# Kernel tuning notes

Measured on AMD Instinct MI355X. Metric: run time of the kernel, lower is better.

## Reference

```python
import jax, jax.numpy as jnp
import numpy as np
from jax.scipy.ndimage import map_coordinates

ANGLES = 180
PROJ = 180
IMG = 256
THETA_RAD = np.deg2rad(np.linspace(0.0, 180.0, ANGLES, endpoint=False)).astype(np.float32)


def _ramp_filter(size):
    # skimage _get_fourier_filter(size, 'ramp')
    n = np.concatenate((np.arange(1, size // 2 + 1, 2),
                        np.arange(size // 2 - 1, 0, -2)))
    f = np.zeros(size)
    f[0] = 0.25
    f[1::2] = -1.0 / (np.pi * n) ** 2
    return (2.0 * np.real(np.fft.fft(f))).astype(np.float32)


def radon_t(img, theta):
    # skimage radon(circle=True): rotate by each angle (bilinear warp) and sum rows
    N = img.shape[0]
    center = N // 2
    y, x = jnp.mgrid[0:N, 0:N]
    x = x.astype(jnp.float32)
    y = y.astype(jnp.float32)

    def one(th):
        c, s = jnp.cos(th), jnp.sin(th)
        sx = c * x + s * y - center * (c + s - 1.0)   # source col
        sy = -s * x + c * y - center * (c - s - 1.0)  # source row
        rot = map_coordinates(img, [sy, sx], order=1, mode='constant', cval=0.0)
        return rot.sum(axis=0)  # sum over rows -> [N]

    cols = jax.vmap(one)(theta)  # [A, N]
    return cols.T                # [N, A] sinogram


def iradon_t(sino, theta):
    # skimage iradon(circle=True, filter='ramp', interpolation='linear')
    N, A = sino.shape
    pad = max(64, int(2 ** np.ceil(np.log2(2 * N))))
    filt = jnp.asarray(_ramp_filter(pad))
    proj = jnp.fft.fft(jnp.pad(sino, ((0, pad - N), (0, 0))), axis=0) * filt[:, None]
    filtered = jnp.real(jnp.fft.ifft(proj, axis=0)[:N, :]).astype(jnp.float32)  # [N, A]

    radius = N // 2
    xpr, ypr = jnp.mgrid[0:N, 0:N]
    xpr = (xpr - radius).astype(jnp.float32)
    ypr = (ypr - radius).astype(jnp.float32)

    def one(col, th):
        # detector coordinate t, shifted so index 0 corresponds to x[0] = -N//2
        t = ypr * jnp.cos(th) - xpr * jnp.sin(th) + radius
        i0 = jnp.floor(t).astype(jnp.int32)
        frac = t - i0
        v0 = col[jnp.clip(i0, 0, N - 1)]
        v1 = col[jnp.clip(i0 + 1, 0, N - 1)]
        val = (1.0 - frac) * v0 + frac * v1
        inb = (t >= 0.0) & (t <= N - 1.0)  # np.interp(..., left=0, right=0)
        return jnp.where(inb, val, 0.0)

    back = jax.vmap(one)(filtered.T, theta).sum(axis=0)  # [N, N]
    mask = (xpr ** 2 + ypr ** 2) <= radius ** 2
    return jnp.where(mask, back, 0.0) * (jnp.pi / (2.0 * A))


def setup_inputs() -> dict:
    key = jax.random.key(0)
    ks = jax.random.split(key, 7)
    scale = 1.0 / np.sqrt(PROJ)
    return {
        "x": jax.random.normal(ks[0], (4, 3, IMG, IMG), dtype=jnp.float32),
        "Wq": jax.random.normal(ks[1], (PROJ, PROJ), dtype=jnp.float32) * scale,
        "bq": jax.random.normal(ks[2], (PROJ,), dtype=jnp.float32) * scale,
        "Wk": jax.random.normal(ks[3], (PROJ, PROJ), dtype=jnp.float32) * scale,
        "bk": jax.random.normal(ks[4], (PROJ,), dtype=jnp.float32) * scale,
        "Wv": jax.random.normal(ks[5], (PROJ, PROJ), dtype=jnp.float32) * scale,
        "bv": jax.random.normal(ks[6], (PROJ,), dtype=jnp.float32) * scale,
    }


def reference(x, Wq, bq, Wk, bk, Wv, bv):
    B, C, H, W = x.shape
    theta = jnp.asarray(THETA_RAD)
    imgs = x.reshape(B * C, H, W)
    sino = jax.vmap(lambda im: radon_t(im, theta))(imgs)  # [BC, H, A]
    Q = sino @ Wq.T + bq
    K = sino @ Wk.T + bk
    V = sino @ Wv.T + bv
    scores = jax.nn.softmax(
        jnp.einsum('nij,nkj->nik', Q, K) / jnp.sqrt(jnp.float32(PROJ)), axis=-1)
    att = jnp.einsum('nik,nkj->nij', scores, V)            # [BC, H, A]
    rec = jax.vmap(lambda s: iradon_t(s, theta))(att)      # [BC, H, W]
    return rec.reshape(B, C, H, W)
```

## Files before the change

### kernel.cpp

```cpp
#include <hip/hip_runtime.h>

#define AANG 180
#define NN 256
#define BCH 12

#ifndef M_PI
#define M_PI 3.14159265358979323846
#endif

__device__ __forceinline__ int iclamp(int v, int lo, int hi) {
    return v < lo ? lo : (v > hi ? hi : v);
}

#define LSTR 259
#define LROWSMAX 130

__global__ __launch_bounds__(1024, 1)
void radon_kernel(const float* __restrict__ x, float* __restrict__ partial) {
    __shared__ float tile[LROWSMAX * LSTR];
    __shared__ float red[2][1024];
    int blk = blockIdx.x;
    int g = blk % 30;
    int t = blk / 30;
    int h = t & 1;
    int n = t >> 1;
    int tid = threadIdx.x;
    int lx = tid & 255;
    int qid = tid >> 8;
    int R0 = h ? 127 : -1;
    int nrows = h ? 130 : 129;
    unsigned lrmax = h ? 128u : 127u;
    const float* img = x + (size_t)n * NN * NN;

    for (int rr = qid; rr < nrows; rr += 4) {
        int gr = R0 + rr;
        bool rok = (gr >= 0) && (gr < NN);
        const float* row = img + gr * NN;
        int gc = lx - 1;
        tile[rr * LSTR + lx] = (rok && gc >= 0) ? row[gc] : 0.0f;
        if (lx < 3) {
            int gc2 = 255 + lx;
            tile[rr * LSTR + 256 + lx] = (rok && gc2 < NN) ? row[gc2] : 0.0f;
        }
    }
    __syncthreads();

    float fx = (float)lx;
    int ubase = qid * 64;

    for (int pp = 0; pp < 3; ++pp) {
        int a0 = g + (2 * pp) * 30;
        int a1 = a0 + 30;
        float th0 = (float)((double)a0 * (M_PI / 180.0));
        float th1 = (float)((double)a1 * (M_PI / 180.0));
        float c0 = cosf(th0), s0 = sinf(th0);
        float c1 = cosf(th1), s1 = sinf(th1);
        float kx0 = -128.0f * (c0 + s0 - 1.0f), ky0 = -128.0f * (c0 - s0 - 1.0f);
        float kx1 = -128.0f * (c1 + s1 - 1.0f), ky1 = -128.0f * (c1 - s1 - 1.0f);
        float xcon0 = c0 * fx + kx0;
        float dcon0 = -s0 * fx + ky0;
        float xcon1 = c1 * fx + kx1;
        float dcon1 = -s1 * fx + ky1;
        float acc0 = 0.0f, acc1 = 0.0f;
#pragma unroll 4
        for (int i = 0; i < 64; ++i) {
            float fy = (float)(ubase + i);
            float sy0 = __builtin_fmaf(c0, fy, dcon0);
            float sx0 = __builtin_fmaf(s0, fy, xcon0);
            float sy1 = __builtin_fmaf(c1, fy, dcon1);
            float sx1 = __builtin_fmaf(s1, fy, xcon1);
            float iyf0 = floorf(sy0), ixf0 = floorf(sx0);
            float iyf1 = floorf(sy1), ixf1 = floorf(sx1);
            int lr0 = (int)iyf0 - R0, lc0 = (int)ixf0 + 1;
            int lr1 = (int)iyf1 - R0, lc1 = (int)ixf1 + 1;
            if ((unsigned)lr0 <= lrmax && (unsigned)lc0 <= 256u) {
                float wy = sy0 - iyf0, wx = sx0 - ixf0;
                const float* t0 = &tile[lr0 * LSTR + lc0];
                float v00 = t0[0], v01 = t0[1];
                float v10 = t0[LSTR], v11 = t0[LSTR + 1];
                float wx1 = 1.0f - wx, wy1 = 1.0f - wy;
                acc0 += wy1 * (wx1 * v00 + wx * v01) + wy * (wx1 * v10 + wx * v11);
            }
            if ((unsigned)lr1 <= lrmax && (unsigned)lc1 <= 256u) {
                float wy = sy1 - iyf1, wx = sx1 - ixf1;
                const float* t1 = &tile[lr1 * LSTR + lc1];
                float v00 = t1[0], v01 = t1[1];
                float v10 = t1[LSTR], v11 = t1[LSTR + 1];
                float wx1 = 1.0f - wx, wy1 = 1.0f - wy;
                acc1 += wy1 * (wx1 * v00 + wx * v01) + wy * (wx1 * v10 + wx * v11);
            }
        }
        if (pp) __syncthreads();
        red[0][tid] = acc0;
        red[1][tid] = acc1;
        __syncthreads();
        if (tid < 256) {
            float r0 = red[0][tid] + red[0][tid + 256] + red[0][tid + 512] + red[0][tid + 768];
            float r1 = red[1][tid] + red[1][tid + 256] + red[1][tid + 512] + red[1][tid + 768];
            size_t base = (((size_t)h * BCH + n) * AANG);
            partial[(base + a0) * NN + tid] = r0;
            partial[(base + a1) * NN + tid] = r1;
        }
    }
}

__global__ void wtrans_kernel(const float* __restrict__ Wq, const float* __restrict__ Wk,
                              const float* __restrict__ Wv, float* __restrict__ WqT,
                              float* __restrict__ WkT, float* __restrict__ WvT) {
    int idx = blockIdx.x * 256 + threadIdx.x;
    if (idx < AANG * AANG) {
        int p = idx / AANG;
        int j = idx - p * AANG;
        int src = j * AANG + p;
        WqT[idx] = Wq[src];
        WkT[idx] = Wk[src];
        WvT[idx] = Wv[src];
    }
}

__global__ void qkv_kernel(const float* __restrict__ partial,
                           const float* __restrict__ WqT, const float* __restrict__ bq,
                           const float* __restrict__ WkT, const float* __restrict__ bk,
                           const float* __restrict__ WvT, const float* __restrict__ bv,
                           float* __restrict__ Q, float* __restrict__ K,
                           float* __restrict__ Vt) {
    __shared__ float srow_t[AANG][8];
    int blk = blockIdx.x;
    int n = blk >> 5;
    int i0 = (blk & 31) * 8;
    int tid = threadIdx.x;
    const size_t HOFF = (size_t)BCH * AANG * NN;
    if (tid < AANG) {
        size_t idx = (((size_t)n) * AANG + tid) * NN + i0;
        float4 p0 = *(const float4*)&partial[idx];
        float4 p1 = *(const float4*)&partial[idx + 4];
        float4 q0 = *(const float4*)&partial[idx + HOFF];
        float4 q1 = *(const float4*)&partial[idx + HOFF + 4];
        srow_t[tid][0] = p0.x + q0.x;
        srow_t[tid][1] = p0.y + q0.y;
        srow_t[tid][2] = p0.z + q0.z;
        srow_t[tid][3] = p0.w + q0.w;
        srow_t[tid][4] = p1.x + q1.x;
        srow_t[tid][5] = p1.y + q1.y;
        srow_t[tid][6] = p1.z + q1.z;
        srow_t[tid][7] = p1.w + q1.w;
    }
    __syncthreads();
    if (tid < AANG) {
        int j = tid;
        float aq[8], ak[8], av[8];
        float bqv = bq[j], bkv = bk[j], bvv = bv[j];
        for (int r = 0; r < 8; ++r) { aq[r] = bqv; ak[r] = bkv; av[r] = bvv; }
#pragma unroll 4
        for (int p = 0; p < AANG; ++p) {
            float wq = WqT[p * AANG + j];
            float wk = WkT[p * AANG + j];
            float wv = WvT[p * AANG + j];
            float4 sv0 = *(const float4*)&srow_t[p][0];
            float4 sv1 = *(const float4*)&srow_t[p][4];
            aq[0] += sv0.x * wq; ak[0] += sv0.x * wk; av[0] += sv0.x * wv;
            aq[1] += sv0.y * wq; ak[1] += sv0.y * wk; av[1] += sv0.y * wv;
            aq[2] += sv0.z * wq; ak[2] += sv0.z * wk; av[2] += sv0.z * wv;
            aq[3] += sv0.w * wq; ak[3] += sv0.w * wk; av[3] += sv0.w * wv;
            aq[4] += sv1.x * wq; ak[4] += sv1.x * wk; av[4] += sv1.x * wv;
            aq[5] += sv1.y * wq; ak[5] += sv1.y * wk; av[5] += sv1.y * wv;
            aq[6] += sv1.z * wq; ak[6] += sv1.z * wk; av[6] += sv1.z * wv;
            aq[7] += sv1.w * wq; ak[7] += sv1.w * wk; av[7] += sv1.w * wv;
        }
        for (int r = 0; r < 8; ++r) {
            size_t qb = ((size_t)(n * NN + i0 + r)) * AANG + j;
            Q[qb] = aq[r];
            K[qb] = ak[r];
        }
        size_t vb = ((size_t)(n * AANG + j)) * NN + i0;
        float4 v0 = make_float4(av[0], av[1], av[2], av[3]);
        float4 v1 = make_float4(av[4], av[5], av[6], av[7]);
        *(float4*)&Vt[vb] = v0;
        *(float4*)&Vt[vb + 4] = v1;
    }
}

__global__ void attn_kernel(const float* __restrict__ Q, const float* __restrict__ K,
                            const float* __restrict__ Vt, float* __restrict__ att_t) {
    __shared__ float qrow[8][AANG];
    __shared__ float prob[8][NN];
    __shared__ float wm[8][4], wsm[8][4];
    int blk = blockIdx.x;
    int n = blk >> 5;
    int i0 = (blk & 31) * 8;
    int tid = threadIdx.x;
    int wid = tid >> 6;
    if (tid < AANG) {
#pragma unroll
        for (int r = 0; r < 8; ++r)
            qrow[r][tid] = Q[((size_t)(n * NN + i0 + r)) * AANG + tid];
    }
    __syncthreads();
    float d[8];
#pragma unroll
    for (int r = 0; r < 8; ++r) d[r] = 0.0f;
    const float* krow = K + ((size_t)(n * NN) + tid) * AANG;
#pragma unroll 3
    for (int jj = 0; jj < AANG / 4; ++jj) {
        float4 kv = *(const float4*)&krow[jj * 4];
#pragma unroll
        for (int r = 0; r < 8; ++r) {
            float4 qv = *(const float4*)&qrow[r][jj * 4];
            d[r] += qv.x * kv.x;
            d[r] += qv.y * kv.y;
            d[r] += qv.z * kv.z;
            d[r] += qv.w * kv.w;
        }
    }
    const float rs = 0.0745355992f;
    float l[8], m[8], e[8], s[8];
#pragma unroll
    for (int r = 0; r < 8; ++r) { l[r] = d[r] * rs; m[r] = l[r]; }
    for (int off = 32; off > 0; off >>= 1) {
#pragma unroll
        for (int r = 0; r < 8; ++r) m[r] = fmaxf(m[r], __shfl_xor(m[r], off));
    }
    if ((tid & 63) == 0) {
#pragma unroll
        for (int r = 0; r < 8; ++r) wm[r][wid] = m[r];
    }
    __syncthreads();
#pragma unroll
    for (int r = 0; r < 8; ++r) {
        float mx = fmaxf(fmaxf(wm[r][0], wm[r][1]), fmaxf(wm[r][2], wm[r][3]));
        e[r] = expf(l[r] - mx);
        s[r] = e[r];
    }
    for (int off = 32; off > 0; off >>= 1) {
#pragma unroll
        for (int r = 0; r < 8; ++r) s[r] += __shfl_xor(s[r], off);
    }
    if ((tid & 63) == 0) {
#pragma unroll
        for (int r = 0; r < 8; ++r) wsm[r][wid] = s[r];
    }
    __syncthreads();
#pragma unroll
    for (int r = 0; r < 8; ++r) {
        float dn = wsm[r][0] + wsm[r][1] + wsm[r][2] + wsm[r][3];
        prob[r][tid] = e[r] / dn;
    }
    __syncthreads();
    if (tid < AANG) {
        float a[8];
#pragma unroll
        for (int r = 0; r < 8; ++r) a[r] = 0.0f;
        const float* vrow = Vt + ((size_t)(n * AANG) + tid) * NN;
#pragma unroll 4
        for (int kk = 0; kk < NN / 4; ++kk) {
            float4 v4 = *(const float4*)&vrow[kk * 4];
#pragma unroll
            for (int r = 0; r < 8; ++r) {
                float4 p4 = *(const float4*)&prob[r][kk * 4];
                a[r] += p4.x * v4.x;
                a[r] += p4.y * v4.y;
                a[r] += p4.z * v4.z;
                a[r] += p4.w * v4.w;
            }
        }
        size_t ob = ((size_t)(n * AANG + tid)) * NN + i0;
        *(float4*)&att_t[ob] = make_float4(a[0], a[1], a[2], a[3]);
        *(float4*)&att_t[ob + 4] = make_float4(a[4], a[5], a[6], a[7]);
    }
}

__global__ void filter_kernel(const float* __restrict__ att_t, float* __restrict__ filt) {
    __shared__ float scol[512];
    __shared__ float coef[128];
    int blk = blockIdx.x;
    int tid = threadIdx.x;
    const float* src = &att_t[(size_t)blk * NN];
    scol[tid] = (tid >= 128) ? src[tid - 128] : 0.0f;
    scol[tid + 256] = (tid < 128) ? src[tid + 128] : 0.0f;
    if (tid < 128) {
        float d = (float)(2 * tid + 1);
        coef[tid] = -2.0f / ((float)(M_PI * M_PI) * d * d);
    }
    __syncthreads();
    const float* c = &scol[tid + 128];
    float acc = 0.5f * c[0];
#pragma unroll 4
    for (int m = 0; m < 128; ++m) {
        int d = 2 * m + 1;
        acc += coef[m] * (c[-d] + c[d]);
    }
    filt[(size_t)blk * NN + tid] = acc;
}

#define ACH 36
__global__ __launch_bounds__(1024)
void backproj_kernel(const float* __restrict__ filt, float* __restrict__ out) {
    __shared__ float cols[ACH][NN];
    __shared__ float cs[AANG], sn[AANG];
    int blk = blockIdx.x;
    int n = blk >> 6;
    int rg = blk & 63;
    int tid = threadIdx.x;
    int col = tid & 255;
    int rslot = tid >> 8;
    int r = rg * 4 + rslot;
    if (tid < AANG) {
        float th = (float)((double)tid * (M_PI / 180.0));
        cs[tid] = cosf(th);
        sn[tid] = sinf(th);
    }
    float xr = (float)(r - 128);
    float yr = (float)(col - 128);
    float acc = 0.0f;
    const float* fb = filt + (size_t)n * AANG * NN;
    for (int ch = 0; ch < AANG / ACH; ++ch) {
        __syncthreads();
        for (int idx = tid; idx < ACH * NN; idx += 1024) {
            int q = idx >> 8;
            int cc = idx & 255;
            cols[q][cc] = fb[(size_t)(ch * ACH + q) * NN + cc];
        }
        __syncthreads();
#pragma unroll 4
        for (int q = 0; q < ACH; ++q) {
            int aa = ch * ACH + q;
            float t = yr * cs[aa] - xr * sn[aa] + 128.0f;
            float i0f = floorf(t);
            int i0 = (int)i0f;
            float frac = t - i0f;
            int c0 = iclamp(i0, 0, NN - 1);
            int c1 = iclamp(i0 + 1, 0, NN - 1);
            float val = (1.0f - frac) * cols[q][c0] + frac * cols[q][c1];
            if (t >= 0.0f && t <= 255.0f) acc += val;
        }
    }
    bool inside = (xr * xr + yr * yr) <= 16384.0f;
    out[((size_t)(n * NN + r)) * NN + col] = inside ? acc * (float)(M_PI / 360.0) : 0.0f;
}

extern "C" void kernel_launch(void* const* d_in, const int* in_sizes, int n_in,
                              void* d_out, int out_size, void* d_ws, size_t ws_size,
                              hipStream_t stream) {
    const float* x  = (const float*)d_in[0];
    const float* Wq = (const float*)d_in[1];
    const float* bq = (const float*)d_in[2];
    const float* Wk = (const float*)d_in[3];
    const float* bk = (const float*)d_in[4];
    const float* Wv = (const float*)d_in[5];
    const float* bv = (const float*)d_in[6];
    float* out = (float*)d_out;
    float* ws = (float*)d_ws;

    const size_t SZ = (size_t)BCH * NN * AANG;
    float* P     = ws;
    float* Q     = P + 2 * SZ;
    float* K     = Q + SZ;
    float* Vt    = K + SZ;
    float* att_t = Vt + SZ;
    float* WqT   = att_t;
    float* WkT   = WqT + AANG * AANG;
    float* WvT   = WkT + AANG * AANG;
    float* filt  = P;

    wtrans_kernel<<<(AANG * AANG + 255) / 256, 256, 0, stream>>>(Wq, Wk, Wv, WqT, WkT, WvT);
    radon_kernel<<<BCH * 2 * 30, 1024, 0, stream>>>(x, P);
    qkv_kernel<<<BCH * (NN / 8), 256, 0, stream>>>(P, WqT, bq, WkT, bk, WvT, bv, Q, K, Vt);
    attn_kernel<<<BCH * (NN / 8), 256, 0, stream>>>(Q, K, Vt, att_t);
    filter_kernel<<<BCH * AANG, NN, 0, stream>>>(att_t, filt);
    backproj_kernel<<<BCH * (NN / 4), 1024, 0, stream>>>(filt, out);
}
```

Before: 448.6 us.

## Fuse all stages into one cooperative persistent kernel with grid syncs

Replaces the six separate launches (weight transpose, radon, QKV, attention, ramp filter, backprojection) with one cooperative kernel of 256 blocks. The stages are separated by grid-wide syncs and share one static LDS buffer. Each stage loops over virtual blocks, and the QKV and attention stages now handle 4 rows per 256-thread sub-block instead of 8. The aim is to remove per-launch overhead and inter-kernel gaps, at the cost of grid.sync latency, possible load imbalance from looping over fixed persistent blocks, and register pressure from the launch bounds of 1024 threads with a minimum of 4 blocks.

```diff
diff --git a/kernel.cpp b/kernel.cpp
--- a/kernel.cpp
+++ b/kernel.cpp
@@ -1,341 +1,362 @@
 #include <hip/hip_runtime.h>
+#include <hip/hip_cooperative_groups.h>
 
 #define AANG 180
 #define NN 256
 #define BCH 12
+#define LSTR 259
+#define LROWSMAX 130
+#define ACH 36
 
 #ifndef M_PI
 #define M_PI 3.14159265358979323846
 #endif
 
+namespace cg = cooperative_groups;
+
 __device__ __forceinline__ int iclamp(int v, int lo, int hi) {
     return v < lo ? lo : (v > hi ? hi : v);
 }
 
-#define LSTR 259
-#define LROWSMAX 130
-
-__global__ __launch_bounds__(1024, 1)
-void radon_kernel(const float* __restrict__ x, float* __restrict__ partial) {
-    __shared__ float tile[LROWSMAX * LSTR];
-    __shared__ float red[2][1024];
-    int blk = blockIdx.x;
-    int g = blk % 30;
-    int t = blk / 30;
-    int h = t & 1;
-    int n = t >> 1;
+#define SMEM_FLOATS (LROWSMAX * LSTR + 2 * 1024)
+
+__global__ __launch_bounds__(1024, 4)
+void fused_kernel(const float* __restrict__ x,
+                  const float* __restrict__ Wq, const float* __restrict__ bq,
+                  const float* __restrict__ Wk, const float* __restrict__ bk,
+                  const float* __restrict__ Wv, const float* __restrict__ bv,
+                  float* __restrict__ out,
+                  float* __restrict__ P, float* __restrict__ Q,
+                  float* __restrict__ K, float* __restrict__ Vt,
+                  float* __restrict__ att_t,
+                  float* __restrict__ WqT, float* __restrict__ WkT,
+                  float* __restrict__ WvT) {
+    __shared__ __align__(16) float smem[SMEM_FLOATS];
+    cg::grid_group grid = cg::this_grid();
     int tid = threadIdx.x;
-    int lx = tid & 255;
-    int qid = tid >> 8;
-    int R0 = h ? 127 : -1;
-    int nrows = h ? 130 : 129;
-    unsigned lrmax = h ? 128u : 127u;
-    const float* img = x + (size_t)n * NN * NN;
-
-    for (int rr = qid; rr < nrows; rr += 4) {
-        int gr = R0 + rr;
-        bool rok = (gr >= 0) && (gr < NN);
-        const float* row = img + gr * NN;
-        int gc = lx - 1;
-        tile[rr * LSTR + lx] = (rok && gc >= 0) ? row[gc] : 0.0f;
-        if (lx < 3) {
-            int gc2 = 255 + lx;
-            tile[rr * LSTR + 256 + lx] = (rok && gc2 < NN) ? row[gc2] : 0.0f;
-        }
-    }
-    __syncthreads();
-
-    float fx = (float)lx;
-    int ubase = qid * 64;
-
-    for (int pp = 0; pp < 3; ++pp) {
-        int a0 = g + (2 * pp) * 30;
-        int a1 = a0 + 30;
-        float th0 = (float)((double)a0 * (M_PI / 180.0));
-        float th1 = (float)((double)a1 * (M_PI / 180.0));
-        float c0 = cosf(th0), s0 = sinf(th0);
-        float c1 = cosf(th1), s1 = sinf(th1);
-        float kx0 = -128.0f * (c0 + s0 - 1.0f), ky0 = -128.0f * (c0 - s0 - 1.0f);
-        float kx1 = -128.0f * (c1 + s1 - 1.0f), ky1 = -128.0f * (c1 - s1 - 1.0f);
-        float xcon0 = c0 * fx + kx0;
-        float dcon0 = -s0 * fx + ky0;
-        float xcon1 = c1 * fx + kx1;
-        float dcon1 = -s1 * fx + ky1;
-        float acc0 = 0.0f, acc1 = 0.0f;
-#pragma unroll 4
-        for (int i = 0; i < 64; ++i) {
-            float fy = (float)(ubase + i);
-            float sy0 = __builtin_fmaf(c0, fy, dcon0);
-            float sx0 = __builtin_fmaf(s0, fy, xcon0);
-            float sy1 = __builtin_fmaf(c1, fy, dcon1);
-            float sx1 = __builtin_fmaf(s1, fy, xcon1);
-            float iyf0 = floorf(sy0), ixf0 = floorf(sx0);
-            float iyf1 = floorf(sy1), ixf1 = floorf(sx1);
-            int lr0 = (int)iyf0 - R0, lc0 = (int)ixf0 + 1;
-            int lr1 = (int)iyf1 - R0, lc1 = (int)ixf1 + 1;
-            if ((unsigned)lr0 <= lrmax && (unsigned)lc0 <= 256u) {
-                float wy = sy0 - iyf0, wx = sx0 - ixf0;
-                const float* t0 = &tile[lr0 * LSTR + lc0];
-                float v00 = t0[0], v01 = t0[1];
-                float v10 = t0[LSTR], v11 = t0[LSTR + 1];
-                float wx1 = 1.0f - wx, wy1 = 1.0f - wy;
-                acc0 += wy1 * (wx1 * v00 + wx * v01) + wy * (wx1 * v10 + wx * v11);
-            }
-            if ((unsigned)lr1 <= lrmax && (unsigned)lc1 <= 256u) {
-                float wy = sy1 - iyf1, wx = sx1 - ixf1;
-                const float* t1 = &tile[lr1 * LSTR + lc1];
-                float v00 = t1[0], v01 = t1[1];
-                float v10 = t1[LSTR], v11 = t1[LSTR + 1];
-                float wx1 = 1.0f - wx, wy1 = 1.0f - wy;
-                acc1 += wy1 * (wx1 * v00 + wx * v01) + wy * (wx1 * v10 + wx * v11);
-            }
-        }
-        if (pp) __syncthreads();
-        red[0][tid] = acc0;
-        red[1][tid] = acc1;
-        __syncthreads();
-        if (tid < 256) {
-            float r0 = red[0][tid] + red[0][tid + 256] + red[0][tid + 512] + red[0][tid + 768];
-            float r1 = red[1][tid] + red[1][tid + 256] + red[1][tid + 512] + red[1][tid + 768];
-            size_t base = (((size_t)h * BCH + n) * AANG);
-            partial[(base + a0) * NN + tid] = r0;
-            partial[(base + a1) * NN + tid] = r1;
-        }
-    }
-}
-
-__global__ void wtrans_kernel(const float* __restrict__ Wq, const float* __restrict__ Wk,
-                              const float* __restrict__ Wv, float* __restrict__ WqT,
-                              float* __restrict__ WkT, float* __restrict__ WvT) {
-    int idx = blockIdx.x * 256 + threadIdx.x;
-    if (idx < AANG * AANG) {
-        int p = idx / AANG;
-        int j = idx - p * AANG;
-        int src = j * AANG + p;
-        WqT[idx] = Wq[src];
-        WkT[idx] = Wk[src];
-        WvT[idx] = Wv[src];
-    }
-}
-
-__global__ void qkv_kernel(const float* __restrict__ partial,
-                           const float* __restrict__ WqT, const float* __restrict__ bq,
-                           const float* __restrict__ WkT, const float* __restrict__ bk,
-                           const float* __restrict__ WvT, const float* __restrict__ bv,
-                           float* __restrict__ Q, float* __restrict__ K,
-                           float* __restrict__ Vt) {
-    __shared__ float srow_t[AANG][8];
-    int blk = blockIdx.x;
-    int n = blk >> 5;
-    int i0 = (blk & 31) * 8;
-    int tid = threadIdx.x;
+    int bid = blockIdx.x;
     const size_t HOFF = (size_t)BCH * AANG * NN;
-    if (tid < AANG) {
-        size_t idx = (((size_t)n) * AANG + tid) * NN + i0;
-        float4 p0 = *(const float4*)&partial[idx];
-        float4 p1 = *(const float4*)&partial[idx + 4];
-        float4 q0 = *(const float4*)&partial[idx + HOFF];
-        float4 q1 = *(const float4*)&partial[idx + HOFF + 4];
-        srow_t[tid][0] = p0.x + q0.x;
-        srow_t[tid][1] = p0.y + q0.y;
-        srow_t[tid][2] = p0.z + q0.z;
-        srow_t[tid][3] = p0.w + q0.w;
-        srow_t[tid][4] = p1.x + q1.x;
-        srow_t[tid][5] = p1.y + q1.y;
-        srow_t[tid][6] = p1.z + q1.z;
-        srow_t[tid][7] = p1.w + q1.w;
-    }
-    __syncthreads();
-    if (tid < AANG) {
-        int j = tid;
-        float aq[8], ak[8], av[8];
-        float bqv = bq[j], bkv = bk[j], bvv = bv[j];
-        for (int r = 0; r < 8; ++r) { aq[r] = bqv; ak[r] = bkv; av[r] = bvv; }
-#pragma unroll 4
-        for (int p = 0; p < AANG; ++p) {
-            float wq = WqT[p * AANG + j];
-            float wk = WkT[p * AANG + j];
-            float wv = WvT[p * AANG + j];
-            float4 sv0 = *(const float4*)&srow_t[p][0];
-            float4 sv1 = *(const float4*)&srow_t[p][4];
-            aq[0] += sv0.x * wq; ak[0] += sv0.x * wk; av[0] += sv0.x * wv;
-            aq[1] += sv0.y * wq; ak[1] += sv0.y * wk; av[1] += sv0.y * wv;
-            aq[2] += sv0.z * wq; ak[2] += sv0.z * wk; av[2] += sv0.z * wv;
-            aq[3] += sv0.w * wq; ak[3] += sv0.w * wk; av[3] += sv0.w * wv;
-            aq[4] += sv1.x * wq; ak[4] += sv1.x * wk; av[4] += sv1.x * wv;
-            aq[5] += sv1.y * wq; ak[5] += sv1.y * wk; av[5] += sv1.y * wv;
-            aq[6] += sv1.z * wq; ak[6] += sv1.z * wk; av[6] += sv1.z * wv;
-            aq[7] += sv1.w * wq; ak[7] += sv1.w * wk; av[7] += sv1.w * wv;
-        }
-        for (int r = 0; r < 8; ++r) {
-            size_t qb = ((size_t)(n * NN + i0 + r)) * AANG + j;
-            Q[qb] = aq[r];
-            K[qb] = ak[r];
-        }
-        size_t vb = ((size_t)(n * AANG + j)) * NN + i0;
-        float4 v0 = make_float4(av[0], av[1], av[2], av[3]);
-        float4 v1 = make_float4(av[4], av[5], av[6], av[7]);
-        *(float4*)&Vt[vb] = v0;
-        *(float4*)&Vt[vb + 4] = v1;
-    }
-}
-
-__global__ void attn_kernel(const float* __restrict__ Q, const float* __restrict__ K,
-                            const float* __restrict__ Vt, float* __restrict__ att_t) {
-    __shared__ float qrow[8][AANG];
-    __shared__ float prob[8][NN];
-    __shared__ float wm[8][4], wsm[8][4];
-    int blk = blockIdx.x;
-    int n = blk >> 5;
-    int i0 = (blk & 31) * 8;
-    int tid = threadIdx.x;
-    int wid = tid >> 6;
-    if (tid < AANG) {
-#pragma unroll
-        for (int r = 0; r < 8; ++r)
-            qrow[r][tid] = Q[((size_t)(n * NN + i0 + r)) * AANG + tid];
-    }
-    __syncthreads();
-    float d[8];
-#pragma unroll
-    for (int r = 0; r < 8; ++r) d[r] = 0.0f;
-    const float* krow = K + ((size_t)(n * NN) + tid) * AANG;
+
+    {
+        int idx = bid * 1024 + tid;
+        if (idx < AANG * AANG) {
+            int p = idx / AANG;
+            int j = idx - p * AANG;
+            int src = j * AANG + p;
+            WqT[idx] = Wq[src];
+            WkT[idx] = Wk[src];
+            WvT[idx] = Wv[src];
+        }
+    }
+    grid.sync();
+
+    {
+        float* tile = smem;
+        float* red0 = smem + LROWSMAX * LSTR;
+        float* red1 = red0 + 1024;
+        int lx = tid & 255;
+        int qid = tid >> 8;
+        float fx = (float)lx;
+        int ubase = qid * 64;
+        for (int vb = bid; vb < BCH * 2 * 30; vb += 256) {
+            __syncthreads();
+            int g = vb % 30;
+            int t = vb / 30;
+            int h = t & 1;
+            int n = t >> 1;
+            int R0 = h ? 127 : -1;
+            int nrows = h ? 130 : 129;
+            unsigned lrmax = h ? 128u : 127u;
+            const float* img = x + (size_t)n * NN * NN;
+            for (int rr = qid; rr < nrows; rr += 4) {
+                int gr = R0 + rr;
+                bool rok = (gr >= 0) && (gr < NN);
+                const float* row = img + gr * NN;
+                int gc = lx - 1;
+                tile[rr * LSTR + lx] = (rok && gc >= 0) ? row[gc] : 0.0f;
+                if (lx < 3) {
+                    int gc2 = 255 + lx;
+                    tile[rr * LSTR + 256 + lx] = (rok && gc2 < NN) ? row[gc2] : 0.0f;
+                }
+            }
+            __syncthreads();
+            for (int pp = 0; pp < 3; ++pp) {
+                int a0 = g + (2 * pp) * 30;
+                int a1 = a0 + 30;
+                float th0 = (float)((double)a0 * (M_PI / 180.0));
+                float th1 = (float)((double)a1 * (M_PI / 180.0));
+                float c0 = cosf(th0), s0 = sinf(th0);
+                float c1 = cosf(th1), s1 = sinf(th1);
+                float kx0 = -128.0f * (c0 + s0 - 1.0f), ky0 = -128.0f * (c0 - s0 - 1.0f);
+                float kx1 = -128.0f * (c1 + s1 - 1.0f), ky1 = -128.0f * (c1 - s1 - 1.0f);
+                float xcon0 = c0 * fx + kx0;
+                float dcon0 = -s0 * fx + ky0;
+                float xcon1 = c1 * fx + kx1;
+                float dcon1 = -s1 * fx + ky1;
+                float acc0 = 0.0f, acc1 = 0.0f;
+#pragma unroll 4
+                for (int i = 0; i < 64; ++i) {
+                    float fy = (float)(ubase + i);
+                    float sy0 = __builtin_fmaf(c0, fy, dcon0);
+                    float sx0 = __builtin_fmaf(s0, fy, xcon0);
+                    float sy1 = __builtin_fmaf(c1, fy, dcon1);
+                    float sx1 = __builtin_fmaf(s1, fy, xcon1);
+                    float iyf0 = floorf(sy0), ixf0 = floorf(sx0);
+                    float iyf1 = floorf(sy1), ixf1 = floorf(sx1);
+                    int lr0 = (int)iyf0 - R0, lc0 = (int)ixf0 + 1;
+                    int lr1 = (int)iyf1 - R0, lc1 = (int)ixf1 + 1;
+                    if ((unsigned)lr0 <= lrmax && (unsigned)lc0 <= 256u) {
+                        float wy = sy0 - iyf0, wx = sx0 - ixf0;
+                        const float* t0 = &tile[lr0 * LSTR + lc0];
+                        float v00 = t0[0], v01 = t0[1];
+                        float v10 = t0[LSTR], v11 = t0[LSTR + 1];
+                        float wx1 = 1.0f - wx, wy1 = 1.0f - wy;
+                        acc0 += wy1 * (wx1 * v00 + wx * v01) + wy * (wx1 * v10 + wx * v11);
+                    }
+                    if ((unsigned)lr1 <= lrmax && (unsigned)lc1 <= 256u) {
+                        float wy = sy1 - iyf1, wx = sx1 - ixf1;
+                        const float* t1 = &tile[lr1 * LSTR + lc1];
+                        float v00 = t1[0], v01 = t1[1];
+                        float v10 = t1[LSTR], v11 = t1[LSTR + 1];
+                        float wx1 = 1.0f - wx, wy1 = 1.0f - wy;
+                        acc1 += wy1 * (wx1 * v00 + wx * v01) + wy * (wx1 * v10 + wx * v11);
+                    }
+                }
+                if (pp) __syncthreads();
+                red0[tid] = acc0;
+                red1[tid] = acc1;
+                __syncthreads();
+                if (tid < 256) {
+                    float r0 = red0[tid] + red0[tid + 256] + red0[tid + 512] + red0[tid + 768];
+                    float r1 = red1[tid] + red1[tid + 256] + red1[tid + 512] + red1[tid + 768];
+                    size_t base = (((size_t)h * BCH + n) * AANG);
+                    P[(base + a0) * NN + tid] = r0;
+                    P[(base + a1) * NN + tid] = r1;
+                }
+            }
+        }
+    }
+    grid.sync();
+
+    {
+        float* srow = smem;
+        int sb = tid >> 8;
+        int t2 = tid & 255;
+        int vb = bid * 4 + sb;
+        bool valid = vb < BCH * 64;
+        int n = vb >> 6;
+        int i0 = (vb & 63) * 4;
+        if (valid && t2 < AANG) {
+            size_t idx = (((size_t)n) * AANG + t2) * NN + i0;
+            float4 p0 = *(const float4*)&P[idx];
+            float4 q0 = *(const float4*)&P[idx + HOFF];
+            float* sr = &srow[(sb * AANG + t2) * 4];
+            sr[0] = p0.x + q0.x;
+            sr[1] = p0.y + q0.y;
+            sr[2] = p0.z + q0.z;
+            sr[3] = p0.w + q0.w;
+        }
+        __syncthreads();
+        if (valid && t2 < AANG) {
+            int j = t2;
+            float aq[4], ak[4], av[4];
+            float bqv = bq[j], bkv = bk[j], bvv = bv[j];
+#pragma unroll
+            for (int r = 0; r < 4; ++r) { aq[r] = bqv; ak[r] = bkv; av[r] = bvv; }
+#pragma unroll 4
+            for (int p = 0; p < AANG; ++p) {
+                float wq = WqT[p * AANG + j];
+                float wk = WkT[p * AANG + j];
+                float wv = WvT[p * AANG + j];
+                float4 sv = *(const float4*)&srow[(sb * AANG + p) * 4];
+                aq[0] += sv.x * wq; ak[0] += sv.x * wk; av[0] += sv.x * wv;
+                aq[1] += sv.y * wq; ak[1] += sv.y * wk; av[1] += sv.y * wv;
+                aq[2] += sv.z * wq; ak[2] += sv.z * wk; av[2] += sv.z * wv;
+                aq[3] += sv.w * wq; ak[3] += sv.w * wk; av[3] += sv.w * wv;
+            }
+#pragma unroll
+            for (int r = 0; r < 4; ++r) {
+                size_t qb = ((size_t)(n * NN + i0 + r)) * AANG + j;
+                Q[qb] = aq[r];
+                K[qb] = ak[r];
+            }
+            size_t vbo = ((size_t)(n * AANG + j)) * NN + i0;
+            *(float4*)&Vt[vbo] = make_float4(av[0], av[1], av[2], av[3]);
+        }
+    }
+    grid.sync();
+
+    {
+        float* qrow = smem;
+        float* prob = smem + 2880;
+        float* wm   = smem + 2880 + 4096;
+        float* wsm  = wm + 64;
+        int sb = tid >> 8;
+        int t2 = tid & 255;
+        int vb = bid * 4 + sb;
+        bool valid = vb < BCH * 64;
+        int n = vb >> 6;
+        int i0 = (vb & 63) * 4;
+        int sw = t2 >> 6;
+        if (valid && t2 < AANG) {
+#pragma unroll
+            for (int r = 0; r < 4; ++r)
+                qrow[(sb * 4 + r) * AANG + t2] = Q[((size_t)(n * NN + i0 + r)) * AANG + t2];
+        }
+        __syncthreads();
+        float d[4] = {0.0f, 0.0f, 0.0f, 0.0f};
+        if (valid) {
+            const float* krow = K + ((size_t)(n * NN) + t2) * AANG;
 #pragma unroll 3
-    for (int jj = 0; jj < AANG / 4; ++jj) {
-        float4 kv = *(const float4*)&krow[jj * 4];
-#pragma unroll
-        for (int r = 0; r < 8; ++r) {
-            float4 qv = *(const float4*)&qrow[r][jj * 4];
-            d[r] += qv.x * kv.x;
-            d[r] += qv.y * kv.y;
-            d[r] += qv.z * kv.z;
-            d[r] += qv.w * kv.w;
-        }
-    }
-    const float rs = 0.0745355992f;
-    float l[8], m[8], e[8], s[8];
-#pragma unroll
-    for (int r = 0; r < 8; ++r) { l[r] = d[r] * rs; m[r] = l[r]; }
-    for (int off = 32; off > 0; off >>= 1) {
-#pragma unroll
-        for (int r = 0; r < 8; ++r) m[r] = fmaxf(m[r], __shfl_xor(m[r], off));
-    }
-    if ((tid & 63) == 0) {
-#pragma unroll
-        for (int r = 0; r < 8; ++r) wm[r][wid] = m[r];
-    }
-    __syncthreads();
-#pragma unroll
-    for (int r = 0; r < 8; ++r) {
-        float mx = fmaxf(fmaxf(wm[r][0], wm[r][1]), fmaxf(wm[r][2], wm[r][3]));
-        e[r] = expf(l[r] - mx);
-        s[r] = e[r];
-    }
-    for (int off = 32; off > 0; off >>= 1) {
-#pragma unroll
-        for (int r = 0; r < 8; ++r) s[r] += __shfl_xor(s[r], off);
-    }
-    if ((tid & 63) == 0) {
-#pragma unroll
-        for (int r = 0; r < 8; ++r) wsm[r][wid] = s[r];
-    }
-    __syncthreads();
-#pragma unroll
-    for (int r = 0; r < 8; ++r) {
-        float dn = wsm[r][0] + wsm[r][1] + wsm[r][2] + wsm[r][3];
-        prob[r][tid] = e[r] / dn;
-    }
-    __syncthreads();
-    if (tid < AANG) {
-        float a[8];
-#pragma unroll
-        for (int r = 0; r < 8; ++r) a[r] = 0.0f;
-        const float* vrow = Vt + ((size_t)(n * AANG) + tid) * NN;
-#pragma unroll 4
-        for (int kk = 0; kk < NN / 4; ++kk) {
-            float4 v4 = *(const float4*)&vrow[kk * 4];
-#pragma unroll
-            for (int r = 0; r < 8; ++r) {
-                float4 p4 = *(const float4*)&prob[r][kk * 4];
-                a[r] += p4.x * v4.x;
-                a[r] += p4.y * v4.y;
-                a[r] += p4.z * v4.z;
-                a[r] += p4.w * v4.w;
-            }
-        }
-        size_t ob = ((size_t)(n * AANG + tid)) * NN + i0;
-        *(float4*)&att_t[ob] = make_float4(a[0], a[1], a[2], a[3]);
-        *(float4*)&att_t[ob + 4] = make_float4(a[4], a[5], a[6], a[7]);
-    }
-}
-
-__global__ void filter_kernel(const float* __restrict__ att_t, float* __restrict__ filt) {
-    __shared__ float scol[512];
-    __shared__ float coef[128];
-    int blk = blockIdx.x;
-    int tid = threadIdx.x;
-    const float* src = &att_t[(size_t)blk * NN];
-    scol[tid] = (tid >= 128) ? src[tid - 128] : 0.0f;
-    scol[tid + 256] = (tid < 128) ? src[tid + 128] : 0.0f;
-    if (tid < 128) {
-        float d = (float)(2 * tid + 1);
-        coef[tid] = -2.0f / ((float)(M_PI * M_PI) * d * d);
-    }
-    __syncthreads();
-    const float* c = &scol[tid + 128];
-    float acc = 0.5f * c[0];
-#pragma unroll 4
-    for (int m = 0; m < 128; ++m) {
-        int d = 2 * m + 1;
-        acc += coef[m] * (c[-d] + c[d]);
-    }
-    filt[(size_t)blk * NN + tid] = acc;
-}
-
-#define ACH 36
-__global__ __launch_bounds__(1024)
-void backproj_kernel(const float* __restrict__ filt, float* __restrict__ out) {
-    __shared__ float cols[ACH][NN];
-    __shared__ float cs[AANG], sn[AANG];
-    int blk = blockIdx.x;
-    int n = blk >> 6;
-    int rg = blk & 63;
-    int tid = threadIdx.x;
-    int col = tid & 255;
-    int rslot = tid >> 8;
-    int r = rg * 4 + rslot;
-    if (tid < AANG) {
-        float th = (float)((double)tid * (M_PI / 180.0));
-        cs[tid] = cosf(th);
-        sn[tid] = sinf(th);
-    }
-    float xr = (float)(r - 128);
-    float yr = (float)(col - 128);
-    float acc = 0.0f;
-    const float* fb = filt + (size_t)n * AANG * NN;
-    for (int ch = 0; ch < AANG / ACH; ++ch) {
-        __syncthreads();
-        for (int idx = tid; idx < ACH * NN; idx += 1024) {
-            int q = idx >> 8;
-            int cc = idx & 255;
-            cols[q][cc] = fb[(size_t)(ch * ACH + q) * NN + cc];
-        }
-        __syncthreads();
-#pragma unroll 4
-        for (int q = 0; q < ACH; ++q) {
-            int aa = ch * ACH + q;
-            float t = yr * cs[aa] - xr * sn[aa] + 128.0f;
-            float i0f = floorf(t);
-            int i0 = (int)i0f;
-            float frac = t - i0f;
-            int c0 = iclamp(i0, 0, NN - 1);
-            int c1 = iclamp(i0 + 1, 0, NN - 1);
-            float val = (1.0f - frac) * cols[q][c0] + frac * cols[q][c1];
-            if (t >= 0.0f && t <= 255.0f) acc += val;
-        }
-    }
-    bool inside = (xr * xr + yr * yr) <= 16384.0f;
-    out[((size_t)(n * NN + r)) * NN + col] = inside ? acc * (float)(M_PI / 360.0) : 0.0f;
+            for (int jj = 0; jj < AANG / 4; ++jj) {
+                float4 kv = *(const float4*)&krow[jj * 4];
+#pragma unroll
+                for (int r = 0; r < 4; ++r) {
+                    float4 qv = *(const float4*)&qrow[(sb * 4 + r) * AANG + jj * 4];
+                    d[r] += qv.x * kv.x;
+                    d[r] += qv.y * kv.y;
+                    d[r] += qv.z * kv.z;
+                    d[r] += qv.w * kv.w;
+                }
+            }
+        }
+        const float rs = 0.0745355992f;
+        float l[4], m[4], e[4], s[4];
+#pragma unroll
+        for (int r = 0; r < 4; ++r) { l[r] = d[r] * rs; m[r] = l[r]; }
+        for (int off = 32; off > 0; off >>= 1) {
+#pragma unroll
+            for (int r = 0; r < 4; ++r) m[r] = fmaxf(m[r], __shfl_xor(m[r], off));
+        }
+        if (valid && (t2 & 63) == 0) {
+#pragma unroll
+            for (int r = 0; r < 4; ++r) wm[(sb * 4 + r) * 4 + sw] = m[r];
+        }
+        __syncthreads();
+#pragma unroll
+        for (int r = 0; r < 4; ++r) {
+            const float* w = &wm[(sb * 4 + r) * 4];
+            float mx = fmaxf(fmaxf(w[0], w[1]), fmaxf(w[2], w[3]));
+            e[r] = expf(l[r] - mx);
+            s[r] = e[r];
+        }
+        for (int off = 32; off > 0; off >>= 1) {
+#pragma unroll
+            for (int r = 0; r < 4; ++r) s[r] += __shfl_xor(s[r], off);
+        }
+        if (valid && (t2 & 63) == 0) {
+#pragma unroll
+            for (int r = 0; r < 4; ++r) wsm[(sb * 4 + r) * 4 + sw] = s[r];
+        }
+        __syncthreads();
+        if (valid) {
+#pragma unroll
+            for (int r = 0; r < 4; ++r) {
+                const float* w = &wsm[(sb * 4 + r) * 4];
+                float dn = w[0] + w[1] + w[2] + w[3];
+                prob[(sb * 4 + r) * NN + t2] = e[r] / dn;
+            }
+        }
+        __syncthreads();
+        if (valid && t2 < AANG) {
+            float a[4] = {0.0f, 0.0f, 0.0f, 0.0f};
+            const float* vrow = Vt + ((size_t)(n * AANG) + t2) * NN;
+#pragma unroll 4
+            for (int kk = 0; kk < NN / 4; ++kk) {
+                float4 v4 = *(const float4*)&vrow[kk * 4];
+#pragma unroll
+                for (int r = 0; r < 4; ++r) {
+                    float4 p4 = *(const float4*)&prob[(sb * 4 + r) * NN + kk * 4];
+                    a[r] += p4.x * v4.x;
+                    a[r] += p4.y * v4.y;
+                    a[r] += p4.z * v4.z;
+                    a[r] += p4.w * v4.w;
+                }
+            }
+            size_t ob = ((size_t)(n * AANG + t2)) * NN + i0;
+            *(float4*)&att_t[ob] = make_float4(a[0], a[1], a[2], a[3]);
+        }
+    }
+    grid.sync();
+
+    {
+        float* coef  = smem;
+        float* scolb = smem + 128;
+        int sb = tid >> 8;
+        int t2 = tid & 255;
+        if (tid < 128) {
+            float dd = (float)(2 * tid + 1);
+            coef[tid] = -2.0f / ((float)(M_PI * M_PI) * dd * dd);
+        }
+        float* scol = scolb + sb * 512;
+        for (int k = 0; k < 3; ++k) {
+            int vb = bid * 4 + sb + k * 1024;
+            bool valid = vb < BCH * AANG;
+            __syncthreads();
+            if (valid) {
+                const float* src = &att_t[(size_t)vb * NN];
+                scol[t2] = (t2 >= 128) ? src[t2 - 128] : 0.0f;
+                scol[t2 + 256] = (t2 < 128) ? src[t2 + 128] : 0.0f;
+            }
+            __syncthreads();
+            if (valid) {
+                const float* c = &scol[t2 + 128];
+                float acc = 0.5f * c[0];
+#pragma unroll 4
+                for (int mm = 0; mm < 128; ++mm) {
+                    int dd = 2 * mm + 1;
+                    acc += coef[mm] * (c[-dd] + c[dd]);
+                }
+                P[(size_t)vb * NN + t2] = acc;
+            }
+        }
+    }
+    grid.sync();
+
+    {
+        float* cols = smem;
+        float* cs   = smem + ACH * NN;
+        float* sn   = cs + AANG;
+        int col = tid & 255;
+        int rslot = tid >> 8;
+        if (tid < AANG) {
+            float th = (float)((double)tid * (M_PI / 180.0));
+            cs[tid] = cosf(th);
+            sn[tid] = sinf(th);
+        }
+        float yr = (float)(col - 128);
+        for (int vb = bid; vb < BCH * 64; vb += 256) {
+            int n = vb >> 6;
+            int rg = vb & 63;
+            int r = rg * 4 + rslot;
+            float xr = (float)(r - 128);
+            float acc = 0.0f;
+            const float* fb = P + (size_t)n * AANG * NN;
+            for (int ch = 0; ch < AANG / ACH; ++ch) {
+                __syncthreads();
+                for (int idx = tid; idx < ACH * NN; idx += 1024) {
+                    int q = idx >> 8;
+                    int cc = idx & 255;
+                    cols[q * NN + cc] = fb[(size_t)(ch * ACH + q) * NN + cc];
+                }
+                __syncthreads();
+#pragma unroll 4
+                for (int q = 0; q < ACH; ++q) {
+                    int aa = ch * ACH + q;
+                    float t = yr * cs[aa] - xr * sn[aa] + 128.0f;
+                    float i0f = floorf(t);
+                    int i0 = (int)i0f;
+                    float frac = t - i0f;
+                    int c0 = iclamp(i0, 0, NN - 1);
+                    int c1 = iclamp(i0 + 1, 0, NN - 1);
+                    float val = (1.0f - frac) * cols[q * NN + c0] + frac * cols[q * NN + c1];
+                    if (t >= 0.0f && t <= 255.0f) acc += val;
+                }
+            }
+            bool inside = (xr * xr + yr * yr) <= 16384.0f;
+            out[((size_t)(n * NN + r)) * NN + col] = inside ? acc * (float)(M_PI / 360.0) : 0.0f;
+        }
+    }
 }
 
 extern "C" void kernel_launch(void* const* d_in, const int* in_sizes, int n_in,
@@ -360,12 +381,13 @@
     float* WqT   = att_t;
     float* WkT   = WqT + AANG * AANG;
     float* WvT   = WkT + AANG * AANG;
-    float* filt  = P;
-
-    wtrans_kernel<<<(AANG * AANG + 255) / 256, 256, 0, stream>>>(Wq, Wk, Wv, WqT, WkT, WvT);
-    radon_kernel<<<BCH * 2 * 30, 1024, 0, stream>>>(x, P);
-    qkv_kernel<<<BCH * (NN / 8), 256, 0, stream>>>(P, WqT, bq, WkT, bk, WvT, bv, Q, K, Vt);
-    attn_kernel<<<BCH * (NN / 8), 256, 0, stream>>>(Q, K, Vt, att_t);
-    filter_kernel<<<BCH * AANG, NN, 0, stream>>>(att_t, filt);
-    backproj_kernel<<<BCH * (NN / 4), 1024, 0, stream>>>(filt, out);
+
+    void* args[] = {
+        (void*)&x, (void*)&Wq, (void*)&bq, (void*)&Wk, (void*)&bk,
+        (void*)&Wv, (void*)&bv, (void*)&out, (void*)&P, (void*)&Q,
+        (void*)&K, (void*)&Vt, (void*)&att_t, (void*)&WqT, (void*)&WkT,
+        (void*)&WvT
+    };
+    hipLaunchCooperativeKernel((void*)fused_kernel, dim3(256), dim3(1024),
+                               args, 0, stream);
 }
```

Result: slower. 631.2 us (+40.7%).

## Fold weight transpose into radon kernel and transpose K/V layouts for coalesced attention

Applied to the files above, without the earlier changes.

The separate weight-transpose launch is removed: each of the 720 radon blocks transposes 45 weight entries before its main work, which saves one kernel launch. K is now stored transposed and V row-major, so in the attention kernel adjacent threads read adjacent addresses with scalar loads. The old layout had each thread issuing strided float4 loads. This trades vector loads for coalesced scalar loads.

```diff
diff --git a/kernel.cpp b/kernel.cpp
--- a/kernel.cpp
+++ b/kernel.cpp
@@ -16,15 +16,29 @@
 #define LROWSMAX 130
 
 __global__ __launch_bounds__(1024, 1)
-void radon_kernel(const float* __restrict__ x, float* __restrict__ partial) {
+void radon_kernel(const float* __restrict__ x, float* __restrict__ partial,
+                  const float* __restrict__ Wq, const float* __restrict__ Wk,
+                  const float* __restrict__ Wv, float* __restrict__ WqT,
+                  float* __restrict__ WkT, float* __restrict__ WvT) {
     __shared__ float tile[LROWSMAX * LSTR];
     __shared__ float red[2][1024];
     int blk = blockIdx.x;
+    int tid = threadIdx.x;
+
+    if (tid < 45) {
+        int idx = blk * 45 + tid;
+        int p = idx / AANG;
+        int j = idx - p * AANG;
+        int src = j * AANG + p;
+        WqT[idx] = Wq[src];
+        WkT[idx] = Wk[src];
+        WvT[idx] = Wv[src];
+    }
+
     int g = blk % 30;
     int t = blk / 30;
     int h = t & 1;
     int n = t >> 1;
-    int tid = threadIdx.x;
     int lx = tid & 255;
     int qid = tid >> 8;
     int R0 = h ? 127 : -1;
@@ -104,26 +118,12 @@
     }
 }
 
-__global__ void wtrans_kernel(const float* __restrict__ Wq, const float* __restrict__ Wk,
-                              const float* __restrict__ Wv, float* __restrict__ WqT,
-                              float* __restrict__ WkT, float* __restrict__ WvT) {
-    int idx = blockIdx.x * 256 + threadIdx.x;
-    if (idx < AANG * AANG) {
-        int p = idx / AANG;
-        int j = idx - p * AANG;
-        int src = j * AANG + p;
-        WqT[idx] = Wq[src];
-        WkT[idx] = Wk[src];
-        WvT[idx] = Wv[src];
-    }
-}
-
 __global__ void qkv_kernel(const float* __restrict__ partial,
                            const float* __restrict__ WqT, const float* __restrict__ bq,
                            const float* __restrict__ WkT, const float* __restrict__ bk,
                            const float* __restrict__ WvT, const float* __restrict__ bv,
-                           float* __restrict__ Q, float* __restrict__ K,
-                           float* __restrict__ Vt) {
+                           float* __restrict__ Q, float* __restrict__ Kt,
+                           float* __restrict__ V) {
     __shared__ float srow_t[AANG][8];
     int blk = blockIdx.x;
     int n = blk >> 5;
@@ -170,18 +170,16 @@
         for (int r = 0; r < 8; ++r) {
             size_t qb = ((size_t)(n * NN + i0 + r)) * AANG + j;
             Q[qb] = aq[r];
-            K[qb] = ak[r];
-        }
-        size_t vb = ((size_t)(n * AANG + j)) * NN + i0;
-        float4 v0 = make_float4(av[0], av[1], av[2], av[3]);
-        float4 v1 = make_float4(av[4], av[5], av[6], av[7]);
-        *(float4*)&Vt[vb] = v0;
-        *(float4*)&Vt[vb + 4] = v1;
-    }
-}
-
-__global__ void attn_kernel(const float* __restrict__ Q, const float* __restrict__ K,
-                            const float* __restrict__ Vt, float* __restrict__ att_t) {
+            V[qb] = av[r];
+        }
+        size_t kb = ((size_t)(n * AANG + j)) * NN + i0;
+        *(float4*)&Kt[kb]     = make_float4(ak[0], ak[1], ak[2], ak[3]);
+        *(float4*)&Kt[kb + 4] = make_float4(ak[4], ak[5], ak[6], ak[7]);
+    }
+}
+
+__global__ void attn_kernel(const float* __restrict__ Q, const float* __restrict__ Kt,
+                            const float* __restrict__ V, float* __restrict__ att_t) {
     __shared__ float qrow[8][AANG];
     __shared__ float prob[8][NN];
     __shared__ float wm[8][4], wsm[8][4];
@@ -199,17 +197,20 @@
     float d[8];
 #pragma unroll
     for (int r = 0; r < 8; ++r) d[r] = 0.0f;
-    const float* krow = K + ((size_t)(n * NN) + tid) * AANG;
+    const float* kcol = Kt + (size_t)n * AANG * NN + tid;
 #pragma unroll 3
     for (int jj = 0; jj < AANG / 4; ++jj) {
-        float4 kv = *(const float4*)&krow[jj * 4];
+        float kv0 = kcol[(size_t)(jj * 4 + 0) * NN];
+        float kv1 = kcol[(size_t)(jj * 4 + 1) * NN];
+        float kv2 = kcol[(size_t)(jj * 4 + 2) * NN];
+        float kv3 = kcol[(size_t)(jj * 4 + 3) * NN];
 #pragma unroll
         for (int r = 0; r < 8; ++r) {
             float4 qv = *(const float4*)&qrow[r][jj * 4];
-            d[r] += qv.x * kv.x;
-            d[r] += qv.y * kv.y;
-            d[r] += qv.z * kv.z;
-            d[r] += qv.w * kv.w;
+            d[r] += qv.x * kv0;
+            d[r] += qv.y * kv1;
+            d[r] += qv.z * kv2;
+            d[r] += qv.w * kv3;
         }
     }
     const float rs = 0.0745355992f;
@@ -250,21 +251,24 @@
         float a[8];
 #pragma unroll
         for (int r = 0; r < 8; ++r) a[r] = 0.0f;
-        const float* vrow = Vt + ((size_t)(n * AANG) + tid) * NN;
+        const float* vcol = V + (size_t)n * NN * AANG + tid;
 #pragma unroll 4
         for (int kk = 0; kk < NN / 4; ++kk) {
-            float4 v4 = *(const float4*)&vrow[kk * 4];
+            float v0 = vcol[(size_t)(kk * 4 + 0) * AANG];
+            float v1 = vcol[(size_t)(kk * 4 + 1) * AANG];
+            float v2 = vcol[(size_t)(kk * 4 + 2) * AANG];
+            float v3 = vcol[(size_t)(kk * 4 + 3) * AANG];
 #pragma unroll
             for (int r = 0; r < 8; ++r) {
                 float4 p4 = *(const float4*)&prob[r][kk * 4];
-                a[r] += p4.x * v4.x;
-                a[r] += p4.y * v4.y;
-                a[r] += p4.z * v4.z;
-                a[r] += p4.w * v4.w;
+                a[r] += p4.x * v0;
+                a[r] += p4.y * v1;
+                a[r] += p4.z * v2;
+                a[r] += p4.w * v3;
             }
         }
         size_t ob = ((size_t)(n * AANG + tid)) * NN + i0;
-        *(float4*)&att_t[ob] = make_float4(a[0], a[1], a[2], a[3]);
+        *(float4*)&att_t[ob]     = make_float4(a[0], a[1], a[2], a[3]);
         *(float4*)&att_t[ob + 4] = make_float4(a[4], a[5], a[6], a[7]);
     }
 }
@@ -354,18 +358,17 @@
     const size_t SZ = (size_t)BCH * NN * AANG;
     float* P     = ws;
     float* Q     = P + 2 * SZ;
-    float* K     = Q + SZ;
-    float* Vt    = K + SZ;
-    float* att_t = Vt + SZ;
+    float* Kt    = Q + SZ;
+    float* V     = Kt + SZ;
+    float* att_t = V + SZ;
     float* WqT   = att_t;
     float* WkT   = WqT + AANG * AANG;
     float* WvT   = WkT + AANG * AANG;
     float* filt  = P;
 
-    wtrans_kernel<<<(AANG * AANG + 255) / 256, 256, 0, stream>>>(Wq, Wk, Wv, WqT, WkT, WvT);
-    radon_kernel<<<BCH * 2 * 30, 1024, 0, stream>>>(x, P);
-    qkv_kernel<<<BCH * (NN / 8), 256, 0, stream>>>(P, WqT, bq, WkT, bk, WvT, bv, Q, K, Vt);
-    attn_kernel<<<BCH * (NN / 8), 256, 0, stream>>>(Q, K, Vt, att_t);
+    radon_kernel<<<BCH * 2 * 30, 1024, 0, stream>>>(x, P, Wq, Wk, Wv, WqT, WkT, WvT);
+    qkv_kernel<<<BCH * (NN / 8), 256, 0, stream>>>(P, WqT, bq, WkT, bk, WvT, bv, Q, Kt, V);
+    attn_kernel<<<BCH * (NN / 8), 256, 0, stream>>>(Q, Kt, V, att_t);
     filter_kernel<<<BCH * AANG, NN, 0, stream>>>(att_t, filt);
     backproj_kernel<<<BCH * (NN / 4), 1024, 0, stream>>>(filt, out);
 }
```

Result: no change. 442.0 us (-1.5%).
